# Kernel tuning notes

Hardware: AMD Instinct MI355X
Metric: run time of the kernel (lower is better)

Reference implementation:

```python
import jax, jax.numpy as jnp
import numpy as np

DIM = 1024
NUM_HEADS = 16
HEAD_DIM = DIM // NUM_HEADS


def setup_inputs() -> dict:
    key = jax.random.key(0)
    k1, k2, k3, k4, k5 = jax.random.split(key, 5)
    s = 0.02
    return {
        "x": jax.random.normal(k1, (2, 2048, DIM), dtype=jnp.float32),
        "Wq": jax.random.normal(k2, (DIM, DIM), dtype=jnp.float32) * s,
        "Wk": jax.random.normal(k3, (DIM, DIM), dtype=jnp.float32) * s,
        "Wv": jax.random.normal(k4, (DIM, DIM), dtype=jnp.float32) * s,
        "Wo": jax.random.normal(k5, (DIM, DIM), dtype=jnp.float32) * s,
    }


def rotate_half(x):
    x1, x2 = x[..., : x.shape[-1] // 2], x[..., x.shape[-1] // 2 :]
    return jnp.concatenate([-x2, x1], axis=-1)


def rope_cos_sin(seq_len, head_dim, dtype):
    inv_freq = 1.0 / (10000.0 ** (jnp.arange(0, head_dim, 2, dtype=jnp.float32) / head_dim))
    t = jnp.arange(seq_len, dtype=jnp.float32)
    freqs = jnp.einsum("i,j->ij", t, inv_freq)  # [S, head_dim/2]
    emb = jnp.concatenate([freqs, freqs], axis=-1)  # [S, head_dim]
    return jnp.cos(emb).astype(dtype), jnp.sin(emb).astype(dtype)


def reference(x, Wq, Wk, Wv, Wo):
    B, S, D = x.shape
    H, Hd = NUM_HEADS, HEAD_DIM
    scale = Hd ** -0.5

    def proj(W):
        # nn.Linear: x @ W.T; reshape to [B, H, S, Hd]
        return (x @ W.T).reshape(B, S, H, Hd).transpose(0, 2, 1, 3)

    q, k, v = proj(Wq), proj(Wk), proj(Wv)
    cos, sin = rope_cos_sin(S, Hd, x.dtype)  # [S, Hd], broadcast over B,H
    q = q * cos + rotate_half(q) * sin
    k = k * cos + rotate_half(k) * sin

    attn = jnp.einsum("bhqd,bhkd->bhqk", q, k) * scale  # [B,H,S,S]
    causal = jnp.triu(jnp.ones((S, S), dtype=bool), k=1)
    attn = jnp.where(causal, -jnp.inf, attn)
    attn = jax.nn.softmax(attn, axis=-1)
    out = jnp.einsum("bhqk,bhkd->bhqd", attn, v)
    out = out.transpose(0, 2, 1, 3).reshape(B, S, D)
    return out @ Wo.T
```

## Files before the change

### kernel.cpp

```cpp
#include <hip/hip_runtime.h>

#define DIM 1024
#define NHEADS 16
#define HD 64
#define SEQ 2048
#define BATCH 2
#define MROWS (BATCH*SEQ)
#define QKVLD 3072

typedef _Float16 h16;
typedef __attribute__((ext_vector_type(2))) _Float16 h16x2;
typedef __attribute__((ext_vector_type(2))) __fp16 fp16x2;
typedef __attribute__((ext_vector_type(4))) _Float16 h16x4;
typedef __attribute__((ext_vector_type(8))) _Float16 h16x8;
typedef __attribute__((ext_vector_type(4))) float f32x4;
typedef __attribute__((ext_vector_type(16))) float f32x16;

union U2 { fp16x2 g; h16x2 h; unsigned u; };

#define CBAR() do { asm volatile("" ::: "memory"); __builtin_amdgcn_s_barrier(); \
                    asm volatile("" ::: "memory"); } while (0)

__global__ __launch_bounds__(256) void prep_k(
    const float* __restrict__ x,  const float* __restrict__ wq,
    const float* __restrict__ wk, const float* __restrict__ wv,
    const float* __restrict__ wo,
    h16* __restrict__ xh, h16* __restrict__ wqkvh, h16* __restrict__ woh,
    float2* __restrict__ rope)
{
    const int NX = MROWS * DIM / 4;
    const int NW = DIM * DIM / 4;
    int gid = blockIdx.x * 256 + threadIdx.x;
    if (gid < NX) {
        float4 v = *reinterpret_cast<const float4*>(x + (size_t)gid * 4);
        h16x4 o; o.x=(h16)v.x; o.y=(h16)v.y; o.z=(h16)v.z; o.w=(h16)v.w;
        *reinterpret_cast<h16x4*>(xh + (size_t)gid * 4) = o;
    } else if (gid < NX + 3 * NW) {
        int j = gid - NX;
        int w = j >> 18, e = j & (NW - 1);
        const float* s = (w == 0) ? wq : (w == 1) ? wk : wv;
        float4 v = *reinterpret_cast<const float4*>(s + (size_t)e * 4);
        h16x4 o; o.x=(h16)v.x; o.y=(h16)v.y; o.z=(h16)v.z; o.w=(h16)v.w;
        *reinterpret_cast<h16x4*>(wqkvh + (size_t)w * DIM * DIM + (size_t)e * 4) = o;
    } else if (gid < NX + 4 * NW) {
        int e = gid - NX - 3 * NW;
        float4 v = *reinterpret_cast<const float4*>(wo + (size_t)e * 4);
        h16x4 o; o.x=(h16)v.x; o.y=(h16)v.y; o.z=(h16)v.z; o.w=(h16)v.w;
        *reinterpret_cast<h16x4*>(woh + (size_t)e * 4) = o;
    } else {
        int t = gid - NX - 4 * NW;
        int s = t >> 5, j = t & 31;
        float inv = powf(10000.0f, -(float)j / 32.0f);
        float ang = (float)s * inv;
        rope[t] = make_float2(cosf(ang), sinf(ang));
    }
}

__global__ __launch_bounds__(512, 1) void gemm256_qkv(
    const h16* __restrict__ A, const h16* __restrict__ Bw,
    h16* __restrict__ C, const float2* __restrict__ rope)
{
    __shared__ h16 As[2][256][64];
    __shared__ h16 Bs[2][256][64];
    const int tid = threadIdx.x, wave = tid >> 6, lane = tid & 63;
    const int lr = lane & 15, lg = lane >> 4;
    const int wm = wave >> 2, wn = wave & 3;
    const int xr = blockIdx.x & 7, jr = blockIdx.x >> 3;
    const int bm = ((xr >> 1) << 2) + (jr & 3);
    const int bn = (xr & 1) * 6 + (jr >> 2);
    const int m0 = bm << 8, n0 = bn << 8;

    const int srl = lane >> 3;
    const int sgc = ((lane & 7) ^ srl) << 3;

#define STAGE_HALF(buf, k0_, h_) do {                                               \
    _Pragma("unroll")                                                               \
    for (int j_ = 0; j_ < 2; ++j_) {                                                \
        int rl_ = ((h_) & 1) * 128 + (j_ * 8 + wave) * 8;                           \
        if ((h_) < 2) {                                                             \
            const h16* g_ = A + (size_t)(m0 + rl_ + srl) * DIM + (k0_) + sgc;       \
            __builtin_amdgcn_global_load_lds(                                       \
                (const __attribute__((address_space(1))) void*)g_,                  \
                (__attribute__((address_space(3))) void*)(&As[buf][rl_][0]), 16, 0, 0); \
        } else {                                                                    \
            const h16* g_ = Bw + (size_t)(n0 + rl_ + srl) * DIM + (k0_) + sgc;      \
            __builtin_amdgcn_global_load_lds(                                       \
                (const __attribute__((address_space(1))) void*)g_,                  \
                (__attribute__((address_space(3))) void*)(&Bs[buf][rl_][0]), 16, 0, 0); \
        }                                                                           \
    }                                                                               \
} while (0)

    f32x4 acc[8][4];
#pragma unroll
    for (int i = 0; i < 8; ++i)
#pragma unroll
        for (int j = 0; j < 4; ++j) acc[i][j] = (f32x4){0.f, 0.f, 0.f, 0.f};

    const int NT = DIM >> 6;
#pragma unroll
    for (int h = 0; h < 4; ++h) STAGE_HALF(0, 0, h);

    int cur = 0;
    for (int t = 0; t < NT; ++t) {
        const int k0n = (t + 1) << 6;
        const bool pf = (t + 1 < NT);
        if (pf) {
#pragma unroll
            for (int h = 0; h < 4; ++h) STAGE_HALF(cur ^ 1, k0n, h);
        }
        if (pf) asm volatile("s_waitcnt vmcnt(8)" ::: "memory");
        else    asm volatile("s_waitcnt vmcnt(0)" ::: "memory");
        CBAR();
        h16x8 bfr[4][2];
#pragma unroll
        for (int ni = 0; ni < 4; ++ni)
#pragma unroll
            for (int ks = 0; ks < 2; ++ks) {
                int r = wn * 64 + ni * 16 + lr;
                int cpos = ((ks << 2) + lg) ^ (lr & 7);
                bfr[ni][ks] = *(const h16x8*)&Bs[cur][r][cpos << 3];
            }
#pragma unroll
        for (int half = 0; half < 2; ++half) {
            h16x8 afr[4][2];
#pragma unroll
            for (int e = 0; e < 4; ++e)
#pragma unroll
                for (int ks = 0; ks < 2; ++ks) {
                    int r = wm * 128 + (half * 4 + e) * 16 + lr;
                    int cpos = ((ks << 2) + lg) ^ (lr & 7);
                    afr[e][ks] = *(const h16x8*)&As[cur][r][cpos << 3];
                }
            __builtin_amdgcn_s_setprio(1);
#pragma unroll
            for (int e = 0; e < 4; ++e)
#pragma unroll
                for (int ni = 0; ni < 4; ++ni)
#pragma unroll
                    for (int ks = 0; ks < 2; ++ks)
                        acc[half * 4 + e][ni] = __builtin_amdgcn_mfma_f32_16x16x32_f16(
                            afr[e][ks], bfr[ni][ks], acc[half * 4 + e][ni], 0, 0, 0);
            __builtin_amdgcn_s_setprio(0);
        }
        CBAR();
        cur ^= 1;
    }
#undef STAGE_HALF

    const int region = n0 >> 10;
    if (region == 2) {
#pragma unroll
        for (int mi = 0; mi < 8; ++mi)
#pragma unroll
            for (int i = 0; i < 4; ++i) {
                int row = m0 + wm * 128 + mi * 16 + lg * 4 + i;
#pragma unroll
                for (int ni = 0; ni < 4; ++ni) {
                    int col = n0 + wn * 64 + ni * 16 + lr;
                    C[(size_t)row * QKVLD + col] = (h16)acc[mi][ni][i];
                }
            }
    } else {
#pragma unroll
        for (int mi = 0; mi < 8; ++mi)
#pragma unroll
            for (int i = 0; i < 4; ++i) {
                int row = m0 + wm * 128 + mi * 16 + lg * 4 + i;
                int s = row & (SEQ - 1);
#pragma unroll
                for (int ni = 0; ni < 4; ++ni) {
                    int col = n0 + wn * 64 + ni * 16 + lr;
                    int d = col & 63;
                    float2 cs = rope[(s << 5) + (d & 31)];
                    float v  = acc[mi][ni][i];
                    float vp = acc[mi][ni ^ 2][i];
                    float rh = (d < 32) ? -vp : vp;
                    C[(size_t)row * QKVLD + col] = (h16)(v * cs.x + rh * cs.y);
                }
            }
    }
}

__global__ __launch_bounds__(256) void gemm_out(
    const h16* __restrict__ A, const h16* __restrict__ Bw,
    float* __restrict__ C, int M, int N, int K)
{
    __shared__ h16 As[2][128][64];
    __shared__ h16 Bs[2][128][64];
    const int tid  = threadIdx.x;
    const int wave = tid >> 6, lane = tid & 63;
    const int lr = lane & 15, lg = lane >> 4;
    const int wm = wave >> 1, wn = wave & 1;
    const int xr = blockIdx.x & 7, jr = blockIdx.x >> 3;
    const int bm = ((xr >> 1) << 3) + (jr & 7);
    const int bn = ((xr & 1) << 2) + (jr >> 3);
    const int m0 = bm << 7, n0 = bn << 7;

    f32x4 acc[4][4];
#pragma unroll
    for (int i = 0; i < 4; ++i)
#pragma unroll
        for (int j = 0; j < 4; ++j) acc[i][j] = (f32x4){0.f, 0.f, 0.f, 0.f};

    const int arow = lane >> 3;
    const int acol = (lane & 7) << 3;

#define GSTAGE(buf, k0_) do {                                                      \
    _Pragma("unroll")                                                              \
    for (int q_ = 0; q_ < 4; ++q_) {                                               \
        int ch_ = wave * 4 + q_;                                                   \
        const h16* ga_ = A + (size_t)(m0 + ch_ * 8 + arow) * K + (k0_) + acol;     \
        __builtin_amdgcn_global_load_lds(                                          \
            (const __attribute__((address_space(1))) void*)ga_,                    \
            (__attribute__((address_space(3))) void*)(&As[buf][ch_ * 8][0]), 16, 0, 0); \
        const h16* gb_ = Bw + (size_t)(n0 + ch_ * 8 + arow) * K + (k0_) + acol;    \
        __builtin_amdgcn_global_load_lds(                                          \
            (const __attribute__((address_space(1))) void*)gb_,                    \
            (__attribute__((address_space(3))) void*)(&Bs[buf][ch_ * 8][0]), 16, 0, 0); \
    }                                                                              \
} while (0)

    const int NT = K >> 6;
    GSTAGE(0, 0);
    int cur = 0;
    for (int t = 0; t < NT; ++t) {
        const bool pf = (t + 1 < NT);
        if (pf) GSTAGE(cur ^ 1, (t + 1) << 6);
        if (pf) asm volatile("s_waitcnt vmcnt(8)" ::: "memory");
        else    asm volatile("s_waitcnt vmcnt(0)" ::: "memory");
        CBAR();
#pragma unroll
        for (int ks = 0; ks < 2; ++ks) {
            h16x8 af[4], bf[4];
#pragma unroll
            for (int mi = 0; mi < 4; ++mi)
                af[mi] = *(const h16x8*)&As[cur][wm * 64 + mi * 16 + lr][ks * 32 + lg * 8];
#pragma unroll
            for (int ni = 0; ni < 4; ++ni)
                bf[ni] = *(const h16x8*)&Bs[cur][wn * 64 + ni * 16 + lr][ks * 32 + lg * 8];
            __builtin_amdgcn_s_setprio(1);
#pragma unroll
            for (int mi = 0; mi < 4; ++mi)
#pragma unroll
                for (int ni = 0; ni < 4; ++ni)
                    acc[mi][ni] = __builtin_amdgcn_mfma_f32_16x16x32_f16(
                        af[mi], bf[ni], acc[mi][ni], 0, 0, 0);
            __builtin_amdgcn_s_setprio(0);
        }
        CBAR();
        cur ^= 1;
    }
#undef GSTAGE

#pragma unroll
    for (int mi = 0; mi < 4; ++mi)
#pragma unroll
        for (int i = 0; i < 4; ++i) {
            int row = m0 + wm * 64 + mi * 16 + lg * 4 + i;
#pragma unroll
            for (int ni = 0; ni < 4; ++ni) {
                int col = n0 + wn * 64 + ni * 16 + lr;
                C[(size_t)row * N + col] = acc[mi][ni][i];
            }
        }
}

__global__ __launch_bounds__(512) void attn_k(
    const h16* __restrict__ QKV, h16* __restrict__ O)
{
    __shared__ h16 Ks[2][64][64];
    __shared__ h16 Vt[2][64][72];

    const int L = blockIdx.x;
    const int j = L >> 3;
    const int bx = j & 7;
    const int by = (L & 7) + ((j >> 3) << 3);
    const int b = by >> 4, h = by & 15;
    const int tid = threadIdx.x, wave = tid >> 6, lane = tid & 63;
    const int lq = lane & 31, hi = lane >> 5;
    const int qlo = bx, qhi = 15 - bx;

    const h16* Qb = QKV + (size_t)b * SEQ * QKVLD + h * HD;
    const h16* Kb = Qb + DIM;
    const h16* Vb = Qb + 2 * DIM;

    const int qw0 = (wave < 4) ? (qlo * 128 + wave * 32)
                               : (qhi * 128 + (wave - 4) * 32);

    h16x8 qf[4];
    {
        const h16* qp = Qb + (size_t)(qw0 + lq) * QKVLD + 8 * hi;
        const h16 qs = (h16)(0.125f * 1.44269504f);
#pragma unroll
        for (int kb = 0; kb < 4; ++kb) {
            qf[kb] = *(const h16x8*)(qp + 16 * kb);
            qf[kb] *= qs;
        }
    }

    float l_run = 0.f;
    f32x16 accd[2];
#pragma unroll
    for (int i = 0; i < 16; ++i) { accd[0][i] = 0.f; accd[1][i] = 0.f; }

    const int kwave = wave - 4;
    const int kr = (tid & 255) >> 3, kc = tid & 7;
    h16x8 vv0, vv1;

#define STAGE_K(bufi, kv0_) do {                                                   \
    const h16* gk0_ = Kb + (size_t)((kv0_) + kr) * QKVLD + ((kc ^ (kr & 7)) << 3); \
    __builtin_amdgcn_global_load_lds(                                              \
        (const __attribute__((address_space(1))) void*)gk0_,                       \
        (__attribute__((address_space(3))) void*)(&Ks[bufi][kwave * 8][0]), 16, 0, 0); \
    const h16* gk1_ = Kb + (size_t)((kv0_) + 32 + kr) * QKVLD + ((kc ^ (kr & 7)) << 3); \
    __builtin_amdgcn_global_load_lds(                                              \
        (const __attribute__((address_space(1))) void*)gk1_,                       \
        (__attribute__((address_space(3))) void*)(&Ks[bufi][32 + kwave * 8][0]), 16, 0, 0); \
} while (0)

#define VLOAD(kv0_) do {                                                           \
    const h16* gv_ = Vb + (size_t)((kv0_) + lane) * QKVLD + 16 * wave;             \
    vv0 = *(const h16x8*)gv_; vv1 = *(const h16x8*)(gv_ + 8);                      \
} while (0)

#define VWRITE(bufi) do {                                                          \
    _Pragma("unroll")                                                              \
    for (int j_ = 0; j_ < 8; ++j_) {                                               \
        Vt[bufi][16 * wave + j_][lane] = vv0[j_];                                  \
        Vt[bufi][16 * wave + 8 + j_][lane] = vv1[j_];                              \
    }                                                                              \
} while (0)

    const int nkv = 2 * qhi + 2;
    if (wave >= 4) STAGE_K(0, 0);
    else { VLOAD(0); VWRITE(0); }
    __syncthreads();

    for (int t = 0; t < nkv; ++t) {
        const int cur = t & 1;
        const int kv0 = t << 6;
        const bool pf = (t + 1 < nkv);
        if (pf) {
            if (wave >= 4) STAGE_K(cur ^ 1, kv0 + 64);
            else VLOAD(kv0 + 64);
        }

        const bool act = (kv0 <= qw0 + 31);
        h16x8 pfrag[4];
        float ls = 0.f;
        if (act) {
            f32x16 s0, s1;
#pragma unroll
            for (int i = 0; i < 16; ++i) { s0[i] = 0.f; s1[i] = 0.f; }
            const int sk = lq & 7;
            __builtin_amdgcn_s_setprio(1);
#pragma unroll
            for (int kb = 0; kb < 4; ++kb) {
                const int ch = ((2 * kb + hi) ^ sk) << 3;
                h16x8 kf0 = *(const h16x8*)&Ks[cur][lq][ch];
                h16x8 kf1 = *(const h16x8*)&Ks[cur][32 + lq][ch];
                s0 = __builtin_amdgcn_mfma_f32_32x32x16_f16(kf0, qf[kb], s0, 0, 0, 0);
                s1 = __builtin_amdgcn_mfma_f32_32x32x16_f16(kf1, qf[kb], s1, 0, 0, 0);
            }
            __builtin_amdgcn_s_setprio(0);
            const bool full = (kv0 + 64 <= qw0);
            float p[32];
            if (full) {
#pragma unroll
                for (int r = 0; r < 16; ++r) {
                    p[r]      = exp2f(s0[r]);
                    p[16 + r] = exp2f(s1[r]);
                }
            } else {
                const int Lq = qw0 + lq - kv0;
#pragma unroll
                for (int r = 0; r < 16; ++r) {
                    const int kvl = (r & 3) + 8 * (r >> 2) + 4 * hi;
                    float e0 = exp2f(s0[r]);
                    float e1 = exp2f(s1[r]);
                    p[r]      = (kvl <= Lq)      ? e0 : 0.f;
                    p[16 + r] = (kvl + 32 <= Lq) ? e1 : 0.f;
                }
            }
            const fp16x2 one2 = {(__fp16)1.0f, (__fp16)1.0f};
#pragma unroll
            for (int kva = 0; kva < 2; ++kva) {
                const int o = 16 * kva;
                U2 x, y, z, w, x2, y2, z2, w2;
                x.g  = __builtin_amdgcn_cvt_pkrtz(p[o+0],  p[o+1]);
                y.g  = __builtin_amdgcn_cvt_pkrtz(p[o+2],  p[o+3]);
                z.g  = __builtin_amdgcn_cvt_pkrtz(p[o+4],  p[o+5]);
                w.g  = __builtin_amdgcn_cvt_pkrtz(p[o+6],  p[o+7]);
                x2.g = __builtin_amdgcn_cvt_pkrtz(p[o+8],  p[o+9]);
                y2.g = __builtin_amdgcn_cvt_pkrtz(p[o+10], p[o+11]);
                z2.g = __builtin_amdgcn_cvt_pkrtz(p[o+12], p[o+13]);
                w2.g = __builtin_amdgcn_cvt_pkrtz(p[o+14], p[o+15]);
#if __has_builtin(__builtin_amdgcn_fdot2)
                ls = __builtin_amdgcn_fdot2(x.g,  one2, ls, false);
                ls = __builtin_amdgcn_fdot2(y.g,  one2, ls, false);
                ls = __builtin_amdgcn_fdot2(z.g,  one2, ls, false);
                ls = __builtin_amdgcn_fdot2(w.g,  one2, ls, false);
                ls = __builtin_amdgcn_fdot2(x2.g, one2, ls, false);
                ls = __builtin_amdgcn_fdot2(y2.g, one2, ls, false);
                ls = __builtin_amdgcn_fdot2(z2.g, one2, ls, false);
                ls = __builtin_amdgcn_fdot2(w2.g, one2, ls, false);
#else
                ls += p[o+0]+p[o+1]+p[o+2]+p[o+3]+p[o+4]+p[o+5]+p[o+6]+p[o+7]
                    + p[o+8]+p[o+9]+p[o+10]+p[o+11]+p[o+12]+p[o+13]+p[o+14]+p[o+15];
#endif
                asm volatile("v_permlane32_swap_b32 %0, %1" : "+v"(x.u),  "+v"(z.u));
                asm volatile("v_permlane32_swap_b32 %0, %1" : "+v"(y.u),  "+v"(w.u));
                asm volatile("v_permlane32_swap_b32 %0, %1" : "+v"(x2.u), "+v"(z2.u));
                asm volatile("v_permlane32_swap_b32 %0, %1" : "+v"(y2.u), "+v"(w2.u));
                h16x8 f0, f1;
                f0[0]=x.h.x;  f0[1]=x.h.y;  f0[2]=y.h.x;  f0[3]=y.h.y;
                f0[4]=z.h.x;  f0[5]=z.h.y;  f0[6]=w.h.x;  f0[7]=w.h.y;
                f1[0]=x2.h.x; f1[1]=x2.h.y; f1[2]=y2.h.x; f1[3]=y2.h.y;
                f1[4]=z2.h.x; f1[5]=z2.h.y; f1[6]=w2.h.x; f1[7]=w2.h.y;
                pfrag[2*kva]   = f0;
                pfrag[2*kva+1] = f1;
            }
            l_run += ls;
        }
        if (pf && wave < 4) VWRITE(cur ^ 1);
        if (act) {
            __builtin_amdgcn_s_setprio(1);
#pragma unroll
            for (int da = 0; da < 2; ++da)
#pragma unroll
                for (int kvb = 0; kvb < 4; ++kvb) {
                    h16x8 vf = *(const h16x8*)&Vt[cur][32 * da + lq][16 * kvb + 8 * hi];
                    accd[da] = __builtin_amdgcn_mfma_f32_32x32x16_f16(vf, pfrag[kvb], accd[da], 0, 0, 0);
                }
            __builtin_amdgcn_s_setprio(0);
        }
        __syncthreads();
    }

    float lt = l_run + __shfl_xor(l_run, 32);
    float inv = 1.0f / lt;
    h16* Ob = O + (size_t)b * SEQ * DIM + h * HD + (size_t)(qw0 + lq) * DIM;
#pragma unroll
    for (int da = 0; da < 2; ++da)
#pragma unroll
        for (int r = 0; r < 16; r += 2) {
            int d = 32 * da + (r & 3) + 8 * (r >> 2) + 4 * hi;
            h16x2 ov;
            ov.x = (h16)(accd[da][r] * inv);
            ov.y = (h16)(accd[da][r + 1] * inv);
            *(h16x2*)(Ob + d) = ov;
        }
#undef STAGE_K
#undef VLOAD
#undef VWRITE
}

extern "C" void kernel_launch(void* const* d_in, const int* in_sizes, int n_in,
                              void* d_out, int out_size, void* d_ws, size_t ws_size,
                              hipStream_t stream)
{
    const float* x  = (const float*)d_in[0];
    const float* Wq = (const float*)d_in[1];
    const float* Wk = (const float*)d_in[2];
    const float* Wv = (const float*)d_in[3];
    const float* Wo = (const float*)d_in[4];

    char* ws = (char*)d_ws;
    h16* xh     = (h16*)(ws);
    h16* wqkvh  = (h16*)(ws + ((size_t)8  << 20));
    h16* woh    = (h16*)(ws + ((size_t)14 << 20));
    h16* QKVd   = (h16*)(ws + ((size_t)16 << 20));
    h16* Od     = (h16*)(ws + ((size_t)40 << 20));
    float2* rope = (float2*)(ws + ((size_t)48 << 20));

    const int NX = MROWS * DIM / 4, NW = DIM * DIM / 4;
    prep_k<<<(NX + 4 * NW + SEQ * 32) / 256, 256, 0, stream>>>(
        x, Wq, Wk, Wv, Wo, xh, wqkvh, woh, rope);

    gemm256_qkv<<<(MROWS / 256) * (QKVLD / 256), 512, 0, stream>>>(
        xh, wqkvh, QKVd, rope);

    attn_k<<<256, 512, 0, stream>>>(QKVd, Od);

    gemm_out<<<(MROWS / 128) * (DIM / 128), 256, 0, stream>>>(
        Od, woh, (float*)d_out, MROWS, DIM, DIM);
}
```

Baseline: 121.7 us.

## Shrink QKV GEMM tiles to 128x128 with 256-thread blocks

Replaces the 256x256-tile, 512-thread QKV projection GEMM with a 128x128-tile, 256-thread kernel, quadrupling the grid so more CUs receive work and per-block LDS/register use drops. The global-to-LDS staging is simplified, and the XOR swizzle on LDS rows is removed. This trades data reuse per tile, and possibly LDS bank conflicts, for better CU occupancy.

```diff
diff --git a/kernel.cpp b/kernel.cpp
--- a/kernel.cpp
+++ b/kernel.cpp
@@ -56,105 +56,84 @@
     }
 }
 
-__global__ __launch_bounds__(512, 1) void gemm256_qkv(
+__global__ __launch_bounds__(256) void gemm_qkv128(
     const h16* __restrict__ A, const h16* __restrict__ Bw,
     h16* __restrict__ C, const float2* __restrict__ rope)
 {
-    __shared__ h16 As[2][256][64];
-    __shared__ h16 Bs[2][256][64];
-    const int tid = threadIdx.x, wave = tid >> 6, lane = tid & 63;
+    __shared__ h16 As[2][128][64];
+    __shared__ h16 Bs[2][128][64];
+    const int tid  = threadIdx.x;
+    const int wave = tid >> 6, lane = tid & 63;
     const int lr = lane & 15, lg = lane >> 4;
-    const int wm = wave >> 2, wn = wave & 3;
+    const int wm = wave >> 1, wn = wave & 1;
     const int xr = blockIdx.x & 7, jr = blockIdx.x >> 3;
-    const int bm = ((xr >> 1) << 2) + (jr & 3);
-    const int bn = (xr & 1) * 6 + (jr >> 2);
-    const int m0 = bm << 8, n0 = bn << 8;
-
-    const int srl = lane >> 3;
-    const int sgc = ((lane & 7) ^ srl) << 3;
-
-#define STAGE_HALF(buf, k0_, h_) do {                                               \
-    _Pragma("unroll")                                                               \
-    for (int j_ = 0; j_ < 2; ++j_) {                                                \
-        int rl_ = ((h_) & 1) * 128 + (j_ * 8 + wave) * 8;                           \
-        if ((h_) < 2) {                                                             \
-            const h16* g_ = A + (size_t)(m0 + rl_ + srl) * DIM + (k0_) + sgc;       \
-            __builtin_amdgcn_global_load_lds(                                       \
-                (const __attribute__((address_space(1))) void*)g_,                  \
-                (__attribute__((address_space(3))) void*)(&As[buf][rl_][0]), 16, 0, 0); \
-        } else {                                                                    \
-            const h16* g_ = Bw + (size_t)(n0 + rl_ + srl) * DIM + (k0_) + sgc;      \
-            __builtin_amdgcn_global_load_lds(                                       \
-                (const __attribute__((address_space(1))) void*)g_,                  \
-                (__attribute__((address_space(3))) void*)(&Bs[buf][rl_][0]), 16, 0, 0); \
-        }                                                                           \
-    }                                                                               \
+    const int bm = ((xr >> 1) << 3) + (jr & 7);
+    const int bn = (xr & 1) * 12 + (jr >> 3);
+    const int m0 = bm << 7, n0 = bn << 7;
+
+    f32x4 acc[4][4];
+#pragma unroll
+    for (int i = 0; i < 4; ++i)
+#pragma unroll
+        for (int j = 0; j < 4; ++j) acc[i][j] = (f32x4){0.f, 0.f, 0.f, 0.f};
+
+    const int arow = lane >> 3;
+    const int acol = (lane & 7) << 3;
+
+#define GSTAGE(buf, k0_) do {                                                      \
+    _Pragma("unroll")                                                              \
+    for (int q_ = 0; q_ < 4; ++q_) {                                               \
+        int ch_ = wave * 4 + q_;                                                   \
+        const h16* ga_ = A + (size_t)(m0 + ch_ * 8 + arow) * DIM + (k0_) + acol;   \
+        __builtin_amdgcn_global_load_lds(                                          \
+            (const __attribute__((address_space(1))) void*)ga_,                    \
+            (__attribute__((address_space(3))) void*)(&As[buf][ch_ * 8][0]), 16, 0, 0); \
+        const h16* gb_ = Bw + (size_t)(n0 + ch_ * 8 + arow) * DIM + (k0_) + acol;  \
+        __builtin_amdgcn_global_load_lds(                                          \
+            (const __attribute__((address_space(1))) void*)gb_,                    \
+            (__attribute__((address_space(3))) void*)(&Bs[buf][ch_ * 8][0]), 16, 0, 0); \
+    }                                                                              \
 } while (0)
 
-    f32x4 acc[8][4];
-#pragma unroll
-    for (int i = 0; i < 8; ++i)
-#pragma unroll
-        for (int j = 0; j < 4; ++j) acc[i][j] = (f32x4){0.f, 0.f, 0.f, 0.f};
-
     const int NT = DIM >> 6;
-#pragma unroll
-    for (int h = 0; h < 4; ++h) STAGE_HALF(0, 0, h);
-
+    GSTAGE(0, 0);
     int cur = 0;
     for (int t = 0; t < NT; ++t) {
-        const int k0n = (t + 1) << 6;
         const bool pf = (t + 1 < NT);
-        if (pf) {
-#pragma unroll
-            for (int h = 0; h < 4; ++h) STAGE_HALF(cur ^ 1, k0n, h);
-        }
+        if (pf) GSTAGE(cur ^ 1, (t + 1) << 6);
         if (pf) asm volatile("s_waitcnt vmcnt(8)" ::: "memory");
         else    asm volatile("s_waitcnt vmcnt(0)" ::: "memory");
         CBAR();
-        h16x8 bfr[4][2];
-#pragma unroll
-        for (int ni = 0; ni < 4; ++ni)
-#pragma unroll
-            for (int ks = 0; ks < 2; ++ks) {
-                int r = wn * 64 + ni * 16 + lr;
-                int cpos = ((ks << 2) + lg) ^ (lr & 7);
-                bfr[ni][ks] = *(const h16x8*)&Bs[cur][r][cpos << 3];
-            }
-#pragma unroll
-        for (int half = 0; half < 2; ++half) {
-            h16x8 afr[4][2];
-#pragma unroll
-            for (int e = 0; e < 4; ++e)
-#pragma unroll
-                for (int ks = 0; ks < 2; ++ks) {
-                    int r = wm * 128 + (half * 4 + e) * 16 + lr;
-                    int cpos = ((ks << 2) + lg) ^ (lr & 7);
-                    afr[e][ks] = *(const h16x8*)&As[cur][r][cpos << 3];
-                }
+#pragma unroll
+        for (int ks = 0; ks < 2; ++ks) {
+            h16x8 af[4], bf[4];
+#pragma unroll
+            for (int mi = 0; mi < 4; ++mi)
+                af[mi] = *(const h16x8*)&As[cur][wm * 64 + mi * 16 + lr][ks * 32 + lg * 8];
+#pragma unroll
+            for (int ni = 0; ni < 4; ++ni)
+                bf[ni] = *(const h16x8*)&Bs[cur][wn * 64 + ni * 16 + lr][ks * 32 + lg * 8];
             __builtin_amdgcn_s_setprio(1);
 #pragma unroll
-            for (int e = 0; e < 4; ++e)
+            for (int mi = 0; mi < 4; ++mi)
 #pragma unroll
                 for (int ni = 0; ni < 4; ++ni)
-#pragma unroll
-                    for (int ks = 0; ks < 2; ++ks)
-                        acc[half * 4 + e][ni] = __builtin_amdgcn_mfma_f32_16x16x32_f16(
-                            afr[e][ks], bfr[ni][ks], acc[half * 4 + e][ni], 0, 0, 0);
+                    acc[mi][ni] = __builtin_amdgcn_mfma_f32_16x16x32_f16(
+                        af[mi], bf[ni], acc[mi][ni], 0, 0, 0);
             __builtin_amdgcn_s_setprio(0);
         }
         CBAR();
         cur ^= 1;
     }
-#undef STAGE_HALF
+#undef GSTAGE
 
     const int region = n0 >> 10;
     if (region == 2) {
 #pragma unroll
-        for (int mi = 0; mi < 8; ++mi)
+        for (int mi = 0; mi < 4; ++mi)
 #pragma unroll
             for (int i = 0; i < 4; ++i) {
-                int row = m0 + wm * 128 + mi * 16 + lg * 4 + i;
+                int row = m0 + wm * 64 + mi * 16 + lg * 4 + i;
 #pragma unroll
                 for (int ni = 0; ni < 4; ++ni) {
                     int col = n0 + wn * 64 + ni * 16 + lr;
@@ -163,10 +142,10 @@
             }
     } else {
 #pragma unroll
-        for (int mi = 0; mi < 8; ++mi)
+        for (int mi = 0; mi < 4; ++mi)
 #pragma unroll
             for (int i = 0; i < 4; ++i) {
-                int row = m0 + wm * 128 + mi * 16 + lg * 4 + i;
+                int row = m0 + wm * 64 + mi * 16 + lg * 4 + i;
                 int s = row & (SEQ - 1);
 #pragma unroll
                 for (int ni = 0; ni < 4; ++ni) {
@@ -478,7 +457,7 @@
     prep_k<<<(NX + 4 * NW + SEQ * 32) / 256, 256, 0, stream>>>(
         x, Wq, Wk, Wv, Wo, xh, wqkvh, woh, rope);
 
-    gemm256_qkv<<<(MROWS / 256) * (QKVLD / 256), 512, 0, stream>>>(
+    gemm_qkv128<<<(MROWS / 128) * (QKVLD / 128), 256, 0, stream>>>(
         xh, wqkvh, QKVd, rope);
 
     attn_k<<<256, 512, 0, stream>>>(QKVd, Od);
```

Result: slower. 130.6 us (+7.3%).
